# Performance work log

Measured on AMD Instinct MI355X. Metric: run time of the kernel, lower is better.

Reference implementation:

```python
import jax, jax.numpy as jnp
import numpy as np

N_NODES = 20000
N_EDGES = 320000
L = 512   # input feature dim (size_dict['small'][0])
D = 256   # hidden dim (feat_channel), heads=1 so head_dim = 256
C = 2     # n_classes


def setup_inputs() -> dict:
    key = jax.random.key(0)
    ks = jax.random.split(key, 18)
    s = 0.02
    inp = {
        "x": jax.random.normal(ks[0], (N_NODES, L), jnp.float32),
        "edge_index": jax.random.randint(ks[1], (2, N_EDGES), 0, N_NODES, dtype=jnp.int32),
        "label": 1,
        # TransformerConv(L, D, heads=1): query/key/value + root skip projections
        "Wq": jax.random.normal(ks[2], (L, D), jnp.float32) * s,
        "bq": jax.random.normal(ks[3], (D,), jnp.float32) * s,
        "Wk": jax.random.normal(ks[4], (L, D), jnp.float32) * s,
        "bk": jax.random.normal(ks[5], (D,), jnp.float32) * s,
        "Wv": jax.random.normal(ks[6], (L, D), jnp.float32) * s,
        "bv": jax.random.normal(ks[7], (D,), jnp.float32) * s,
        "Ws": jax.random.normal(ks[8], (L, D), jnp.float32) * s,
        "bs": jax.random.normal(ks[9], (D,), jnp.float32) * s,
        # GlobalAdaptPooling: tanh-MLP attention (heads = n_classes) + per-class classifier
        "Wa1": jax.random.normal(ks[10], (D, D), jnp.float32) * s,
        "ba1": jax.random.normal(ks[11], (D,), jnp.float32) * s,
        "Wa2": jax.random.normal(ks[12], (D, C), jnp.float32) * s,
        "ba2": jax.random.normal(ks[13], (C,), jnp.float32) * s,
        "Wc": jax.random.normal(ks[14], (C, D), jnp.float32) * s,
        "bc": jax.random.normal(ks[15], (C,), jnp.float32) * s,
    }
    return inp


def _forward(x, edge_index, label, Wq, bq, Wk, bk, Wv, bv, Ws, bs, Wa1, ba1, Wa2, ba2, Wc, bc):
    n = x.shape[0]
    src = edge_index[0]  # message source j
    dst = edge_index[1]  # message target i
    # --- TransformerConv (heads=1, concat, root_weight=True) ---
    q = x @ Wq + bq                      # [N, D]
    k = x @ Wk + bk
    v = x @ Wv + bv
    score = jnp.sum(q[dst] * k[src], axis=-1) / jnp.sqrt(jnp.float32(D))  # [E]
    # segment softmax over incoming edges of each target node
    m = jax.ops.segment_max(score, dst, num_segments=n)
    e = jnp.exp(score - m[dst])
    den = jax.ops.segment_sum(e, dst, num_segments=n)
    alpha = e / den[dst]                 # [E]
    agg = jax.ops.segment_sum(alpha[:, None] * v[src], dst, num_segments=n)  # [N, D]
    h = agg + x @ Ws + bs
    # --- act: GELU (torch exact/erf) ---
    h = jax.nn.gelu(h, approximate=False)
    # --- GlobalAdaptPooling: node attention with n_classes heads ---
    scores = jnp.tanh(h @ Wa1 + ba1) @ Wa2 + ba2      # [N, C]
    attn = jax.nn.softmax(scores, axis=0)             # softmax over nodes
    M = attn.T @ h                                    # [C, D] per-class bag embedding
    logits = (jnp.sum(M * Wc, axis=1) + bc)[None, :]  # [1, C]
    Y_prob = jax.nn.softmax(logits, axis=1)
    A = attn[:, label]                                # [N] attention for target class
    return logits, Y_prob, A


def reference(x, edge_index, label, Wq, bq, Wk, bk, Wv, bv, Ws, bs, Wa1, ba1, Wa2, ba2, Wc, bc):
    return _forward(x, edge_index, label, Wq, bq, Wk, bk, Wv, bv, Ws, bs, Wa1, ba1, Wa2, ba2, Wc, bc)
```

## Files before the change

kernel.cpp:

```cpp
#include <hip/hip_runtime.h>
#include <hip/hip_bf16.h>
#include <math.h>

typedef float f32x4_t __attribute__((ext_vector_type(4)));
typedef float f32x2_t __attribute__((ext_vector_type(2)));
typedef __bf16 bf16x8_t __attribute__((ext_vector_type(8)));

__device__ __forceinline__ float bf2f(unsigned int u){
  union { float f; unsigned int i; } x; x.i = u << 16; return x.f;
}
__device__ __forceinline__ unsigned short f2bf(float f){
  unsigned int x = __float_as_uint(f);
  unsigned int r = (x + 0x7fffu + ((x >> 16) & 1u)) >> 16;
  return (unsigned short)r;
}
__device__ __forceinline__ unsigned int pk2bf(float a, float b){
  return (unsigned int)f2bf(a) | ((unsigned int)f2bf(b) << 16);
}
__device__ __forceinline__ int swz4(int r){ return (r ^ (r >> 2) ^ (r >> 4)) & 3; }

__device__ __forceinline__ void unp8s(uint4 w, float* f, float s){
  f[0] = bf2f(w.x & 0xffffu) * s; f[1] = bf2f(w.x >> 16) * s;
  f[2] = bf2f(w.y & 0xffffu) * s; f[3] = bf2f(w.y >> 16) * s;
  f[4] = bf2f(w.z & 0xffffu) * s; f[5] = bf2f(w.z >> 16) * s;
  f[6] = bf2f(w.w & 0xffffu) * s; f[7] = bf2f(w.w >> 16) * s;
}
__device__ __forceinline__ void unpf8(unsigned int w, float* f){
  f32x2_t lo = __builtin_amdgcn_cvt_pk_f32_fp8(w, false);
  f32x2_t hi = __builtin_amdgcn_cvt_pk_f32_fp8(w, true);
  f[0] = lo[0]; f[1] = lo[1]; f[2] = hi[0]; f[3] = hi[1];
}
__device__ __forceinline__ float fast_tanh(float y){
  float e = exp2f(y * 2.8853901817f);
  return 1.0f - 2.0f / (e + 1.0f);
}
__device__ __forceinline__ float fast_gelu(float x){
  float x2 = x * x;
  float u = x * fmaf(0.1029527f, x2, 2.3022339f);
  float e = exp2f(u);
  return x - x / (e + 1.0f);
}

#define GLOAD16(gsrc, ldst) \
  __builtin_amdgcn_global_load_lds((const __attribute__((address_space(1))) unsigned int*)(gsrc), \
                                   (__attribute__((address_space(3))) unsigned int*)(ldst), 16, 0, 0)

__global__ void zero_buf(uint4* __restrict__ p, int n16){
  int i = blockIdx.x * 256 + threadIdx.x;
  if (i < n16) p[i] = make_uint4(0, 0, 0, 0);
}

__global__ void prep(const float* __restrict__ x,
                     const float* __restrict__ Wq, const float* __restrict__ Wk,
                     const float* __restrict__ Wv, const float* __restrict__ Ws,
                     const float* __restrict__ bq, const float* __restrict__ bk,
                     const float* __restrict__ bv, const float* __restrict__ bs,
                     const float* __restrict__ Wa1, const int* __restrict__ ei,
                     unsigned short* __restrict__ xbf, unsigned short* __restrict__ wcatT,
                     float* __restrict__ bcat, unsigned short* __restrict__ wa1T,
                     int* __restrict__ deg, int n, int ne, int nbcv){
  const int b = blockIdx.x, tid = threadIdx.x;
  if (b < 2048){
    int idx = b * 256 + tid;
    int c = idx >> 9, k = idx & 511;
    int sel = c >> 8, cc = c & 255;
    const float* W = (sel == 0) ? Wq : (sel == 1) ? Wk : (sel == 2) ? Wv : Ws;
    int p = ((k >> 3) & 3) ^ swz4(c & 127);
    int dst = c * 512 + (k & ~31) + p * 8 + (k & 7);
    wcatT[dst] = f2bf(W[k * 256 + cc]);
    if (idx < 1024){
      int sel2 = idx >> 8, cc2 = idx & 255;
      const float* B = (sel2 == 0) ? bq : (sel2 == 1) ? bk : (sel2 == 2) ? bv : bs;
      bcat[idx] = B[cc2];
    }
  } else if (b < 2304){
    int idx = (b - 2048) * 256 + tid;
    int c = idx >> 8, k = idx & 255;
    wa1T[idx] = f2bf(Wa1[k * 256 + c]);
  } else if (b < 2304 + nbcv){
    int idx = (b - 2304) * 256 + tid;
    if (idx < n * 64){
      int node = idx >> 6, un = idx & 63;
      int k0 = (un >> 2) * 32, u = un & 3;
      const float* src = x + (size_t)node * 512 + k0 + u * 8;
      float4 f0 = *reinterpret_cast<const float4*>(src);
      float4 f1 = *reinterpret_cast<const float4*>(src + 4);
      uint4 o;
      o.x = pk2bf(f0.x, f0.y); o.y = pk2bf(f0.z, f0.w);
      o.z = pk2bf(f1.x, f1.y); o.w = pk2bf(f1.z, f1.w);
      int p = u ^ swz4(node & 127);
      *reinterpret_cast<uint4*>(xbf + (size_t)node * 512 + k0 + p * 8) = o;
    }
  } else {
    int i = (b - 2304 - nbcv) * 256 + tid;
    if (i < ne) atomicAdd(&deg[ei[ne + i]], 1);
  }
}

__global__ __launch_bounds__(256) void gemm_qkvs(const unsigned short* __restrict__ xbf,
                                                 const unsigned short* __restrict__ wcatT,
                                                 const float* __restrict__ bcat,
                                                 unsigned short* __restrict__ qbf,
                                                 unsigned short* __restrict__ sbf,
                                                 unsigned char* __restrict__ kv8,
                                                 int n_nodes, int mblocks){
  __shared__ __align__(16) unsigned char smem[49152];
  const int tid = threadIdx.x;
  const int lane = tid & 63, wave = tid >> 6;
  const int wm = wave >> 1, wn = wave & 1;
  const int g = (blockIdx.x & 7) * mblocks + (blockIdx.x >> 3);
  const int m_blk = g >> 3, n_blk = g & 7;
  const int m0 = m_blk * 128, n0 = n_blk * 128;
  const int lrow = lane >> 2;
  const int lcol = (lane & 3) * 8;
  const int rA0 = min(m0 + wave * 16 + lrow, n_nodes - 1);
  const int rA1 = min(m0 + (wave + 4) * 16 + lrow, n_nodes - 1);
  const int rB0 = n0 + wave * 16 + lrow;
  const int rB1 = rB0 + 64;
  const int r = lane & 15, q4 = lane >> 4;
  const unsigned short* aG0 = xbf   + (size_t)rA0 * 512 + lcol;
  const unsigned short* aG1 = xbf   + (size_t)rA1 * 512 + lcol;
  const unsigned short* bG0 = wcatT + (size_t)rB0 * 512 + lcol;
  const unsigned short* bG1 = wcatT + (size_t)rB1 * 512 + lcol;
  int aoff[4], boff[4];
  #pragma unroll
  for (int mi = 0; mi < 4; mi++){ int rr = wm * 64 + mi * 16 + r; aoff[mi] = rr * 32 + ((q4 ^ swz4(rr)) * 8); }
  #pragma unroll
  for (int ni = 0; ni < 4; ni++){ int rb = wn * 64 + ni * 16 + r; boff[ni] = rb * 32 + ((q4 ^ swz4(rb)) * 8); }
  f32x4_t acc[4][4] = {};
#define STAGE(base, k0) { \
    unsigned short* As_ = (unsigned short*)(smem + (base)); \
    unsigned short* Bs_ = (unsigned short*)(smem + (base) + 8192); \
    GLOAD16(aG0 + (k0), &As_[wave * 512]); \
    GLOAD16(aG1 + (k0), &As_[(wave + 4) * 512]); \
    GLOAD16(bG0 + (k0), &Bs_[wave * 512]); \
    GLOAD16(bG1 + (k0), &Bs_[(wave + 4) * 512]); \
  }
  STAGE(0, 0);
  STAGE(16384, 32);
  int cbase = 0;
  int sbase = 32768;
  for (int t = 0; t < 16; t++){
    if (t + 2 < 16){
      STAGE(sbase, (t + 2) * 32);
      asm volatile("s_waitcnt vmcnt(8)" ::: "memory");
    } else if (t + 1 < 16){
      asm volatile("s_waitcnt vmcnt(4)" ::: "memory");
    } else {
      asm volatile("s_waitcnt vmcnt(0)" ::: "memory");
    }
    __builtin_amdgcn_s_barrier();
    asm volatile("" ::: "memory");
    const unsigned short* As = (const unsigned short*)(smem + cbase);
    const unsigned short* Bs = (const unsigned short*)(smem + cbase + 8192);
    bf16x8_t a[4], b[4];
    #pragma unroll
    for (int mi = 0; mi < 4; mi++) a[mi] = *reinterpret_cast<const bf16x8_t*>(&As[aoff[mi]]);
    #pragma unroll
    for (int ni = 0; ni < 4; ni++) b[ni] = *reinterpret_cast<const bf16x8_t*>(&Bs[boff[ni]]);
    #pragma unroll
    for (int mi = 0; mi < 4; mi++)
      #pragma unroll
      for (int ni = 0; ni < 4; ni++)
        acc[mi][ni] = __builtin_amdgcn_mfma_f32_16x16x32_bf16(b[ni], a[mi], acc[mi][ni], 0, 0, 0);
    __builtin_amdgcn_s_barrier();
    asm volatile("" ::: "memory");
    cbase += 16384; if (cbase == 49152) cbase = 0;
    sbase += 16384; if (sbase == 49152) sbase = 0;
  }
#undef STAGE
  const bool isQ = (n_blk < 2), isS = (n_blk >= 6);
  if (isQ || isS){
    unsigned short* St = (unsigned short*)smem;
    unsigned short* outp = isQ ? qbf : sbf;
    const int colhalf = isQ ? n_blk : (n_blk - 6);
    #pragma unroll
    for (int ch = 0; ch < 2; ch++){
      if (wm == ch){
        #pragma unroll
        for (int mi = 0; mi < 4; mi++){
          #pragma unroll
          for (int ni = 0; ni < 4; ni++){
            int mloc = mi * 16 + r;
            int nl = wn * 64 + ni * 16 + q4 * 4;
            float4 bb = *reinterpret_cast<const float4*>(&bcat[n0 + nl]);
            uint2 w;
            w.x = pk2bf(acc[mi][ni][0] + bb.x, acc[mi][ni][1] + bb.y);
            w.y = pk2bf(acc[mi][ni][2] + bb.z, acc[mi][ni][3] + bb.w);
            *reinterpret_cast<uint2*>(&St[mloc * 152 + nl]) = w;
          }
        }
      }
      __syncthreads();
      #pragma unroll
      for (int it = 0; it < 4; it++){
        int u = it * 256 + tid;
        int row = u >> 4, seg = (u & 15) * 8;
        int node = m0 + ch * 64 + row;
        if (node < n_nodes){
          uint4 v = *reinterpret_cast<const uint4*>(&St[row * 152 + seg]);
          *reinterpret_cast<uint4*>(outp + (size_t)node * 256 + colhalf * 128 + seg) = v;
        }
      }
      __syncthreads();
    }
  } else {
    unsigned char* St8 = smem;
    #pragma unroll
    for (int ch = 0; ch < 2; ch++){
      if (wm == ch){
        #pragma unroll
        for (int mi = 0; mi < 4; mi++){
          #pragma unroll
          for (int ni = 0; ni < 4; ni++){
            int mloc = mi * 16 + r;
            int nl = wn * 64 + ni * 16 + q4 * 4;
            float4 bb = *reinterpret_cast<const float4*>(&bcat[n0 + nl]);
            int u = 0;
            u = __builtin_amdgcn_cvt_pk_fp8_f32(acc[mi][ni][0] + bb.x, acc[mi][ni][1] + bb.y, u, false);
            u = __builtin_amdgcn_cvt_pk_fp8_f32(acc[mi][ni][2] + bb.z, acc[mi][ni][3] + bb.w, u, true);
            *reinterpret_cast<unsigned int*>(&St8[mloc * 144 + nl]) = (unsigned int)u;
          }
        }
      }
      __syncthreads();
      #pragma unroll
      for (int it = 0; it < 2; it++){
        int u = it * 256 + tid;
        int row = u >> 3, seg = (u & 7) * 16;
        int node = m0 + ch * 64 + row;
        if (node < n_nodes){
          uint4 v = *reinterpret_cast<const uint4*>(&St8[row * 144 + seg]);
          *reinterpret_cast<uint4*>(kv8 + (size_t)node * 512 + (n_blk - 2) * 128 + seg) = v;
        }
      }
      __syncthreads();
    }
  }
}

__global__ void scan_deg(const int* __restrict__ deg, int* __restrict__ rowstart, int n, int ne){
  __shared__ int sm[1024];
  int tid = threadIdx.x;
  int per = (n + 1023) / 1024;
  int start = tid * per;
  int sum = 0;
  for (int i = 0; i < per; i++){
    int idx = start + i;
    sum += (idx < n) ? deg[idx] : 0;
  }
  sm[tid] = sum; __syncthreads();
  for (int off = 1; off < 1024; off <<= 1){
    int t = (tid >= off) ? sm[tid - off] : 0;
    __syncthreads();
    sm[tid] += t;
    __syncthreads();
  }
  int run = sm[tid] - sum;
  for (int i = 0; i < per; i++){
    int idx = start + i;
    if (idx < n){
      rowstart[idx] = run;
      run += deg[idx];
    }
  }
  if (tid == 0) rowstart[n] = ne;
}

__global__ void scatter_edges(const int* __restrict__ ei, const int* __restrict__ rowstart,
                              int* __restrict__ cursor, int* __restrict__ csrsrc, int ne){
  int i = blockIdx.x * 256 + threadIdx.x;
  if (i < ne){
    int d = ei[ne + i];
    int pos = atomicAdd(&cursor[d], 1);
    csrsrc[rowstart[d] + pos] = ei[i] << 9;
  }
}

__global__ __launch_bounds__(256) void edge_attn(const unsigned short* __restrict__ qbf,
                                                 const unsigned short* __restrict__ sbf,
                                                 const unsigned char* __restrict__ kv8,
                                                 const int* __restrict__ rowstart,
                                                 const int* __restrict__ csrsrc,
                                                 unsigned short* __restrict__ hbf, int n_nodes){
  const int tid = threadIdx.x;
  const int lane = tid & 63, wave = tid >> 6;
  const int g = lane >> 4, t = lane & 15;
  const int chain = g & 1;
  const int node = blockIdx.x * 8 + wave * 2 + (g >> 1);
  const bool active = node < n_nodes;
  const int nd = active ? node : 0;
  const float qs = 0.0625f * 1.44269504088896340736f;
  float q[16];
  {
    const unsigned short* qp = qbf + (size_t)nd * 256 + t * 16;
    uint4 w0 = *reinterpret_cast<const uint4*>(qp);
    uint4 w1 = *reinterpret_cast<const uint4*>(qp + 8);
    unp8s(w0, q, qs); unp8s(w1, q + 8, qs);
  }
  int rs = rowstart[nd];
  int re = active ? rowstart[nd + 1] : rs;
  float m = -1e30f, den = 0.f;
  float acc[16];
  #pragma unroll
  for (int j = 0; j < 16; j++) acc[j] = 0.f;
  const int i0 = rs + chain;
  uint4 kA = make_uint4(0,0,0,0), vA = kA, kB = kA, vB = kA;
  if (i0 < re){
    const unsigned char* p1 = kv8 + (size_t)csrsrc[i0] + t * 16;
    kA = *reinterpret_cast<const uint4*>(p1);
    vA = *reinterpret_cast<const uint4*>(p1 + 256);
    if (i0 + 2 < re){
      const unsigned char* p2 = kv8 + (size_t)csrsrc[i0 + 2] + t * 16;
      kB = *reinterpret_cast<const uint4*>(p2);
      vB = *reinterpret_cast<const uint4*>(p2 + 256);
    }
  }
  for (int i = i0; i < re; i += 4){
    uint4 k1 = kA, v1 = vA, k2 = kB, v2 = vB;
    const bool has2 = (i + 2 < re);
    if (i + 4 < re){
      const unsigned char* p1 = kv8 + (size_t)csrsrc[i + 4] + t * 16;
      kA = *reinterpret_cast<const uint4*>(p1);
      vA = *reinterpret_cast<const uint4*>(p1 + 256);
      if (i + 6 < re){
        const unsigned char* p2 = kv8 + (size_t)csrsrc[i + 6] + t * 16;
        kB = *reinterpret_cast<const uint4*>(p2);
        vB = *reinterpret_cast<const uint4*>(p2 + 256);
      }
    }
    float kf1[16], kf2[16];
    unpf8(k1.x, kf1); unpf8(k1.y, kf1 + 4); unpf8(k1.z, kf1 + 8); unpf8(k1.w, kf1 + 12);
    unpf8(k2.x, kf2); unpf8(k2.y, kf2 + 4); unpf8(k2.z, kf2 + 8); unpf8(k2.w, kf2 + 12);
    float s1 = 0.f, s2 = 0.f;
    #pragma unroll
    for (int j = 0; j < 16; j++){ s1 = fmaf(q[j], kf1[j], s1); s2 = fmaf(q[j], kf2[j], s2); }
    s1 += __shfl_xor(s1, 1); s2 += __shfl_xor(s2, 1);
    s1 += __shfl_xor(s1, 2); s2 += __shfl_xor(s2, 2);
    s1 += __shfl_xor(s1, 4); s2 += __shfl_xor(s2, 4);
    s1 += __shfl_xor(s1, 8); s2 += __shfl_xor(s2, 8);
    if (!has2) s2 = -1e30f;
    float vf1[16], vf2[16];
    unpf8(v1.x, vf1); unpf8(v1.y, vf1 + 4); unpf8(v1.z, vf1 + 8); unpf8(v1.w, vf1 + 12);
    unpf8(v2.x, vf2); unpf8(v2.y, vf2 + 4); unpf8(v2.z, vf2 + 8); unpf8(v2.w, vf2 + 12);
    float mn = fmaxf(m, fmaxf(s1, s2));
    float sc = exp2f(m - mn);
    float e1 = exp2f(s1 - mn);
    float e2 = exp2f(s2 - mn);
    den = den * sc + e1 + e2;
    #pragma unroll
    for (int j = 0; j < 16; j++)
      acc[j] = fmaf(acc[j], sc, fmaf(e1, vf1[j], e2 * vf2[j]));
    m = mn;
  }
  {
    float mo  = __shfl_xor(m, 16);
    float dno = __shfl_xor(den, 16);
    float mn  = fmaxf(m, mo);
    float a_  = exp2f(m - mn);
    float b_  = exp2f(mo - mn);
    den = den * a_ + dno * b_;
    #pragma unroll
    for (int j = 0; j < 16; j++){
      float oth = __shfl_xor(acc[j], 16);
      acc[j] = acc[j] * a_ + oth * b_;
    }
  }
  float inv = (den > 0.f) ? 1.f / den : 0.f;
  const unsigned short* sp = sbf + (size_t)nd * 256 + t * 16;
  uint4 s0 = *reinterpret_cast<const uint4*>(sp);
  uint4 s1v = *reinterpret_cast<const uint4*>(sp + 8);
  float sf[16]; unp8s(s0, sf, 1.0f); unp8s(s1v, sf + 8, 1.0f);
  unsigned int o[8];
  #pragma unroll
  for (int j = 0; j < 8; j++){
    float h0 = fast_gelu(acc[2 * j] * inv + sf[2 * j]);
    float h1 = fast_gelu(acc[2 * j + 1] * inv + sf[2 * j + 1]);
    o[j] = (unsigned int)f2bf(h0) | ((unsigned int)f2bf(h1) << 16);
  }
  if (active && chain == 0){
    uint4* dst = reinterpret_cast<uint4*>(hbf + (size_t)node * 256 + t * 16);
    dst[0] = make_uint4(o[0], o[1], o[2], o[3]);
    dst[1] = make_uint4(o[4], o[5], o[6], o[7]);
  }
}

__global__ __launch_bounds__(256) void mlp_mfma(const unsigned short* __restrict__ hbf,
                                                const unsigned short* __restrict__ wa1T,
                                                const float* __restrict__ ba1,
                                                const float* __restrict__ Wa2,
                                                const float* __restrict__ ba2,
                                                float* __restrict__ s2, int n_nodes){
  __shared__ __align__(16) unsigned short As[64 * 72];
  __shared__ float s2s[64][2];
  const int tid = threadIdx.x;
  const int lane = tid & 63, wave = tid >> 6;
  const int m0 = blockIdx.x * 64;
  const int c0 = wave * 64;
  const int r = lane & 15, rg = (lane >> 4) * 4;
  if (tid < 128) s2s[tid >> 1][tid & 1] = 0.f;
  f32x4_t acc[4][4] = {};
  for (int k0 = 0; k0 < 256; k0 += 64){
    int arow = tid >> 2, akc = (tid & 3) * 16;
    uint4 a0v = make_uint4(0,0,0,0), a1v = make_uint4(0,0,0,0);
    if (m0 + arow < n_nodes){
      const unsigned short* src = hbf + (size_t)(m0 + arow) * 256 + k0 + akc;
      a0v = *reinterpret_cast<const uint4*>(src);
      a1v = *reinterpret_cast<const uint4*>(src + 8);
    }
    *reinterpret_cast<uint4*>(&As[arow * 72 + akc]) = a0v;
    *reinterpret_cast<uint4*>(&As[arow * 72 + akc + 8]) = a1v;
    __syncthreads();
    #pragma unroll
    for (int kk = 0; kk < 2; kk++){
      int kg = kk * 32 + (lane >> 4) * 8;
      bf16x8_t a[4], b[4];
      #pragma unroll
      for (int mi = 0; mi < 4; mi++)
        a[mi] = *reinterpret_cast<const bf16x8_t*>(&As[(mi * 16 + r) * 72 + kg]);
      #pragma unroll
      for (int ni = 0; ni < 4; ni++)
        b[ni] = *reinterpret_cast<const bf16x8_t*>(wa1T + (size_t)(c0 + ni * 16 + r) * 256 + k0 + kg);
      #pragma unroll
      for (int mi = 0; mi < 4; mi++)
        #pragma unroll
        for (int ni = 0; ni < 4; ni++)
          acc[mi][ni] = __builtin_amdgcn_mfma_f32_16x16x32_bf16(a[mi], b[ni], acc[mi][ni], 0, 0, 0);
    }
    __syncthreads();
  }
  float w20[4], w21[4], b1c[4];
  #pragma unroll
  for (int ni = 0; ni < 4; ni++){
    int col = c0 + ni * 16 + r;
    w20[ni] = Wa2[col * 2]; w21[ni] = Wa2[col * 2 + 1]; b1c[ni] = ba1[col];
  }
  #pragma unroll
  for (int mi = 0; mi < 4; mi++){
    #pragma unroll
    for (int j = 0; j < 4; j++){
      float t0 = 0.f, t1 = 0.f;
      #pragma unroll
      for (int ni = 0; ni < 4; ni++){
        float t = fast_tanh(acc[mi][ni][j] + b1c[ni]);
        t0 += t * w20[ni]; t1 += t * w21[ni];
      }
      t0 += __shfl_xor(t0, 1); t0 += __shfl_xor(t0, 2);
      t0 += __shfl_xor(t0, 4); t0 += __shfl_xor(t0, 8);
      t1 += __shfl_xor(t1, 1); t1 += __shfl_xor(t1, 2);
      t1 += __shfl_xor(t1, 4); t1 += __shfl_xor(t1, 8);
      if (r == 0){
        int row = mi * 16 + rg + j;
        atomicAdd(&s2s[row][0], t0);
        atomicAdd(&s2s[row][1], t1);
      }
    }
  }
  __syncthreads();
  if (tid < 128){
    int row = tid >> 1, c = tid & 1;
    int node = m0 + row;
    if (node < n_nodes) s2[node * 2 + c] = s2s[row][c] + ba2[c];
  }
}

__global__ void col_reduce(const float* __restrict__ s2, float* __restrict__ red, int n){
  __shared__ float sm[1024];
  __shared__ float mshare[2];
  int tid = threadIdx.x;
  float mx0 = -INFINITY, mx1 = -INFINITY;
  for (int i = tid; i < n; i += 1024){
    mx0 = fmaxf(mx0, s2[2 * i]);
    mx1 = fmaxf(mx1, s2[2 * i + 1]);
  }
  sm[tid] = mx0; __syncthreads();
  for (int off = 512; off > 0; off >>= 1){
    if (tid < off) sm[tid] = fmaxf(sm[tid], sm[tid + off]);
    __syncthreads();
  }
  if (tid == 0) mshare[0] = sm[0];
  __syncthreads();
  sm[tid] = mx1; __syncthreads();
  for (int off = 512; off > 0; off >>= 1){
    if (tid < off) sm[tid] = fmaxf(sm[tid], sm[tid + off]);
    __syncthreads();
  }
  if (tid == 0) mshare[1] = sm[0];
  __syncthreads();
  float m0 = mshare[0], m1 = mshare[1];
  float s0 = 0.f, s1 = 0.f;
  for (int i = tid; i < n; i += 1024){
    s0 += expf(s2[2 * i] - m0);
    s1 += expf(s2[2 * i + 1] - m1);
  }
  sm[tid] = s0; __syncthreads();
  for (int off = 512; off > 0; off >>= 1){
    if (tid < off) sm[tid] += sm[tid + off];
    __syncthreads();
  }
  float den0 = sm[0];
  __syncthreads();
  sm[tid] = s1; __syncthreads();
  for (int off = 512; off > 0; off >>= 1){
    if (tid < off) sm[tid] += sm[tid + off];
    __syncthreads();
  }
  if (tid == 0){
    red[0] = m0; red[1] = m1; red[2] = den0; red[3] = sm[0];
  }
}

__global__ __launch_bounds__(256) void attn_M(const float* __restrict__ s2, const float* __restrict__ red,
                                              const unsigned short* __restrict__ hbf, const int* __restrict__ label,
                                              float* __restrict__ Mbuf, float* __restrict__ outA, int n){
  __shared__ float a0s[256], a1s[256];
  __shared__ float Ms[512];
  int tid = threadIdx.x;
  int n0 = blockIdx.x * 256;
  int node = n0 + tid;
  float m0 = red[0], m1 = red[1];
  float i0 = 1.f / red[2], i1 = 1.f / red[3];
  float a0 = 0.f, a1 = 0.f;
  if (node < n){
    a0 = expf(s2[2 * node] - m0) * i0;
    a1 = expf(s2[2 * node + 1] - m1) * i1;
    outA[node] = (label[0] == 0) ? a0 : a1;
  }
  a0s[tid] = a0; a1s[tid] = a1;
  Ms[tid] = 0.f; Ms[tid + 256] = 0.f;
  __syncthreads();
  const int dgrp = tid & 31;
  const int nl = tid >> 5;
  float M0[8] = {}, M1[8] = {};
  for (int i = nl; i < 256; i += 8){
    int nd = n0 + i;
    if (nd >= n) break;
    uint4 w = *reinterpret_cast<const uint4*>(hbf + (size_t)nd * 256 + dgrp * 8);
    float f[8]; unp8s(w, f, 1.0f);
    float A0 = a0s[i], A1 = a1s[i];
    #pragma unroll
    for (int j = 0; j < 8; j++){
      M0[j] = fmaf(A0, f[j], M0[j]);
      M1[j] = fmaf(A1, f[j], M1[j]);
    }
  }
  #pragma unroll
  for (int j = 0; j < 8; j++){
    M0[j] += __shfl_xor(M0[j], 32);
    M1[j] += __shfl_xor(M1[j], 32);
  }
  if ((tid & 32) == 0){
    #pragma unroll
    for (int j = 0; j < 8; j++){
      atomicAdd(&Ms[dgrp * 8 + j], M0[j]);
      atomicAdd(&Ms[256 + dgrp * 8 + j], M1[j]);
    }
  }
  __syncthreads();
  atomicAdd(&Mbuf[tid], Ms[tid]);
  atomicAdd(&Mbuf[256 + tid], Ms[tid + 256]);
}

__global__ void final_k(const float* __restrict__ Mbuf, const float* __restrict__ Wc,
                        const float* __restrict__ bc, float* __restrict__ out){
  __shared__ float sm[256];
  __shared__ float l0s;
  int tid = threadIdx.x;
  float p0 = Mbuf[tid] * Wc[tid];
  float p1 = Mbuf[256 + tid] * Wc[256 + tid];
  sm[tid] = p0; __syncthreads();
  for (int off = 128; off > 0; off >>= 1){
    if (tid < off) sm[tid] += sm[tid + off];
    __syncthreads();
  }
  if (tid == 0) l0s = sm[0];
  __syncthreads();
  sm[tid] = p1; __syncthreads();
  for (int off = 128; off > 0; off >>= 1){
    if (tid < off) sm[tid] += sm[tid + off];
    __syncthreads();
  }
  if (tid == 0){
    float l0 = l0s + bc[0];
    float l1 = sm[0] + bc[1];
    out[0] = l0; out[1] = l1;
    float mx = fmaxf(l0, l1);
    float e0 = expf(l0 - mx), e1 = expf(l1 - mx);
    float inv = 1.f / (e0 + e1);
    out[2] = e0 * inv; out[3] = e1 * inv;
  }
}

extern "C" void kernel_launch(void* const* d_in, const int* in_sizes, int n_in,
                              void* d_out, int out_size, void* d_ws, size_t ws_size,
                              hipStream_t stream) {
  const float* x   = (const float*)d_in[0];
  const int*   ei  = (const int*)d_in[1];
  const int*   lab = (const int*)d_in[2];
  const float* Wq  = (const float*)d_in[3];
  const float* bq  = (const float*)d_in[4];
  const float* Wk  = (const float*)d_in[5];
  const float* bk  = (const float*)d_in[6];
  const float* Wv  = (const float*)d_in[7];
  const float* bv  = (const float*)d_in[8];
  const float* Ws  = (const float*)d_in[9];
  const float* bs  = (const float*)d_in[10];
  const float* Wa1 = (const float*)d_in[11];
  const float* ba1 = (const float*)d_in[12];
  const float* Wa2 = (const float*)d_in[13];
  const float* ba2 = (const float*)d_in[14];
  const float* Wc  = (const float*)d_in[15];
  const float* bc  = (const float*)d_in[16];
  float* out = (float*)d_out;

  const int n  = in_sizes[0] / 512;
  const int ne = in_sizes[1] / 2;

  char* ws = (char*)d_ws;
  size_t off = 0;
  auto take = [&](size_t bytes){ size_t r = off; off += (bytes + 255) & ~(size_t)255; return r; };
  unsigned short* wcatT  = (unsigned short*)(ws + take((size_t)1024 * 512 * 2));
  float*          bcat   = (float*)(ws + take(1024 * 4));
  unsigned short* xbf    = (unsigned short*)(ws + take((size_t)n * 512 * 2));
  unsigned short* qbf    = (unsigned short*)(ws + take((size_t)n * 256 * 2));
  unsigned short* sbf    = (unsigned short*)(ws + take((size_t)n * 256 * 2));
  unsigned char*  kv8    = (unsigned char*)(ws + take((size_t)n * 512));
  unsigned short* hbf    = (unsigned short*)(ws + take((size_t)n * 256 * 2));
  unsigned short* wa1T   = (unsigned short*)(ws + take((size_t)256 * 256 * 2));
  float*          s2     = (float*)(ws + take((size_t)n * 2 * 4));
  size_t zoff = off;
  int*            deg    = (int*)(ws + take((size_t)n * 4));
  int*            cursor = (int*)(ws + take((size_t)n * 4));
  float*          Mbuf   = (float*)(ws + take(512 * 4));
  size_t zlen = off - zoff;
  int*            rowst  = (int*)(ws + take((size_t)(n + 1) * 4));
  int*            csrsrc = (int*)(ws + take((size_t)ne * 4));
  float*          red    = (float*)(ws + take(4 * 4));

  const int z16 = (int)(zlen / 16);
  zero_buf<<<(z16 + 255) / 256, 256, 0, stream>>>((uint4*)(ws + zoff), z16);

  const int nbcv = (n * 64 + 255) / 256;
  const int nbdh = (ne + 255) / 256;
  prep<<<2304 + nbcv + nbdh, 256, 0, stream>>>(x, Wq, Wk, Wv, Ws, bq, bk, bv, bs, Wa1, ei,
                                               xbf, wcatT, bcat, wa1T, deg, n, ne, nbcv);
  const int mblocks = (n + 127) / 128;
  gemm_qkvs<<<8 * mblocks, 256, 0, stream>>>(xbf, wcatT, bcat, qbf, sbf, kv8, n, mblocks);
  scan_deg<<<1, 1024, 0, stream>>>(deg, rowst, n, ne);
  scatter_edges<<<(ne + 255) / 256, 256, 0, stream>>>(ei, rowst, cursor, csrsrc, ne);
  edge_attn<<<(n + 7) / 8, 256, 0, stream>>>(qbf, sbf, kv8, rowst, csrsrc, hbf, n);
  mlp_mfma<<<(n + 63) / 64, 256, 0, stream>>>(hbf, wa1T, ba1, Wa2, ba2, s2, n);
  col_reduce<<<1, 1024, 0, stream>>>(s2, red, n);
  attn_M<<<(n + 255) / 256, 256, 0, stream>>>(s2, red, hbf, lab, Mbuf, out + 4, n);
  final_k<<<1, 256, 0, stream>>>(Mbuf, Wc, bc, out);
  (void)ws_size; (void)out_size; (void)n_in;
}
```

Baseline: 197.5 us.

## Drop max-subtraction in node softmax and fuse reductions into neighbor kernels

The mlp_mfma epilogue now computes exp of the per-node class scores directly, with no global max, and accumulates the softmax denominators through wave shuffles and global atomics. This removes the single-block col_reduce kernel. The final_k classifier is folded into attn_M with a last-block-done counter, saving two launches and a serial one-block pass. The cost is exp without max-subtraction, which could overflow for large scores (safe here only because the tanh-bounded scores are small), plus atomic and order-dependent summation of the denominators.

```diff
diff --git a/kernel.cpp b/kernel.cpp
--- a/kernel.cpp
+++ b/kernel.cpp
@@ -390,7 +390,8 @@
                                                 const float* __restrict__ ba1,
                                                 const float* __restrict__ Wa2,
                                                 const float* __restrict__ ba2,
-                                                float* __restrict__ s2, int n_nodes){
+                                                float* __restrict__ es2,
+                                                float* __restrict__ den_g, int n_nodes){
   __shared__ __align__(16) unsigned short As[64 * 72];
   __shared__ float s2s[64][2];
   const int tid = threadIdx.x;
@@ -460,70 +461,36 @@
   if (tid < 128){
     int row = tid >> 1, c = tid & 1;
     int node = m0 + row;
-    if (node < n_nodes) s2[node * 2 + c] = s2s[row][c] + ba2[c];
-  }
-}
-
-__global__ void col_reduce(const float* __restrict__ s2, float* __restrict__ red, int n){
-  __shared__ float sm[1024];
-  __shared__ float mshare[2];
-  int tid = threadIdx.x;
-  float mx0 = -INFINITY, mx1 = -INFINITY;
-  for (int i = tid; i < n; i += 1024){
-    mx0 = fmaxf(mx0, s2[2 * i]);
-    mx1 = fmaxf(mx1, s2[2 * i + 1]);
-  }
-  sm[tid] = mx0; __syncthreads();
-  for (int off = 512; off > 0; off >>= 1){
-    if (tid < off) sm[tid] = fmaxf(sm[tid], sm[tid + off]);
-    __syncthreads();
-  }
-  if (tid == 0) mshare[0] = sm[0];
-  __syncthreads();
-  sm[tid] = mx1; __syncthreads();
-  for (int off = 512; off > 0; off >>= 1){
-    if (tid < off) sm[tid] = fmaxf(sm[tid], sm[tid + off]);
-    __syncthreads();
-  }
-  if (tid == 0) mshare[1] = sm[0];
-  __syncthreads();
-  float m0 = mshare[0], m1 = mshare[1];
-  float s0 = 0.f, s1 = 0.f;
-  for (int i = tid; i < n; i += 1024){
-    s0 += expf(s2[2 * i] - m0);
-    s1 += expf(s2[2 * i + 1] - m1);
-  }
-  sm[tid] = s0; __syncthreads();
-  for (int off = 512; off > 0; off >>= 1){
-    if (tid < off) sm[tid] += sm[tid + off];
-    __syncthreads();
-  }
-  float den0 = sm[0];
-  __syncthreads();
-  sm[tid] = s1; __syncthreads();
-  for (int off = 512; off > 0; off >>= 1){
-    if (tid < off) sm[tid] += sm[tid + off];
-    __syncthreads();
-  }
-  if (tid == 0){
-    red[0] = m0; red[1] = m1; red[2] = den0; red[3] = sm[0];
-  }
-}
-
-__global__ __launch_bounds__(256) void attn_M(const float* __restrict__ s2, const float* __restrict__ red,
+    float e = 0.f;
+    if (node < n_nodes){
+      e = expf(s2s[row][c] + ba2[c]);
+      es2[node * 2 + c] = e;
+    }
+    float sum = e;
+    sum += __shfl_xor(sum, 2);  sum += __shfl_xor(sum, 4);
+    sum += __shfl_xor(sum, 8);  sum += __shfl_xor(sum, 16);
+    sum += __shfl_xor(sum, 32);
+    if ((tid & 63) < 2) atomicAdd(&den_g[c], sum);
+  }
+}
+
+__global__ __launch_bounds__(256) void attn_M(const float* __restrict__ es2, const float* __restrict__ den_g,
                                               const unsigned short* __restrict__ hbf, const int* __restrict__ label,
-                                              float* __restrict__ Mbuf, float* __restrict__ outA, int n){
+                                              float* __restrict__ Mbuf, float* __restrict__ outA,
+                                              const float* __restrict__ Wc, const float* __restrict__ bc,
+                                              float* __restrict__ out, unsigned int* __restrict__ cnt,
+                                              int n, int nblocks){
   __shared__ float a0s[256], a1s[256];
   __shared__ float Ms[512];
+  __shared__ unsigned int lastrank;
   int tid = threadIdx.x;
   int n0 = blockIdx.x * 256;
   int node = n0 + tid;
-  float m0 = red[0], m1 = red[1];
-  float i0 = 1.f / red[2], i1 = 1.f / red[3];
+  float i0 = 1.f / den_g[0], i1 = 1.f / den_g[1];
   float a0 = 0.f, a1 = 0.f;
   if (node < n){
-    a0 = expf(s2[2 * node] - m0) * i0;
-    a1 = expf(s2[2 * node + 1] - m1) * i1;
+    a0 = es2[2 * node] * i0;
+    a1 = es2[2 * node + 1] * i1;
     outA[node] = (label[0] == 0) ? a0 : a1;
   }
   a0s[tid] = a0; a1s[tid] = a1;
@@ -559,35 +526,28 @@
   __syncthreads();
   atomicAdd(&Mbuf[tid], Ms[tid]);
   atomicAdd(&Mbuf[256 + tid], Ms[tid + 256]);
-}
-
-__global__ void final_k(const float* __restrict__ Mbuf, const float* __restrict__ Wc,
-                        const float* __restrict__ bc, float* __restrict__ out){
-  __shared__ float sm[256];
-  __shared__ float l0s;
-  int tid = threadIdx.x;
-  float p0 = Mbuf[tid] * Wc[tid];
-  float p1 = Mbuf[256 + tid] * Wc[256 + tid];
-  sm[tid] = p0; __syncthreads();
-  for (int off = 128; off > 0; off >>= 1){
-    if (tid < off) sm[tid] += sm[tid + off];
+  __threadfence();
+  if (tid == 0) lastrank = atomicAdd(cnt, 1u);
+  __syncthreads();
+  if (lastrank == (unsigned int)(nblocks - 1)){
+    float m0v = __hip_atomic_load(&Mbuf[tid], __ATOMIC_RELAXED, __HIP_MEMORY_SCOPE_AGENT);
+    float m1v = __hip_atomic_load(&Mbuf[256 + tid], __ATOMIC_RELAXED, __HIP_MEMORY_SCOPE_AGENT);
+    a0s[tid] = m0v * Wc[tid];
+    a1s[tid] = m1v * Wc[256 + tid];
     __syncthreads();
-  }
-  if (tid == 0) l0s = sm[0];
-  __syncthreads();
-  sm[tid] = p1; __syncthreads();
-  for (int off = 128; off > 0; off >>= 1){
-    if (tid < off) sm[tid] += sm[tid + off];
-    __syncthreads();
-  }
-  if (tid == 0){
-    float l0 = l0s + bc[0];
-    float l1 = sm[0] + bc[1];
-    out[0] = l0; out[1] = l1;
-    float mx = fmaxf(l0, l1);
-    float e0 = expf(l0 - mx), e1 = expf(l1 - mx);
-    float inv = 1.f / (e0 + e1);
-    out[2] = e0 * inv; out[3] = e1 * inv;
+    for (int off = 128; off > 0; off >>= 1){
+      if (tid < off){ a0s[tid] += a0s[tid + off]; a1s[tid] += a1s[tid + off]; }
+      __syncthreads();
+    }
+    if (tid == 0){
+      float l0 = a0s[0] + bc[0];
+      float l1 = a1s[0] + bc[1];
+      out[0] = l0; out[1] = l1;
+      float mx = fmaxf(l0, l1);
+      float e0 = expf(l0 - mx), e1 = expf(l1 - mx);
+      float inv = 1.f / (e0 + e1);
+      out[2] = e0 * inv; out[3] = e1 * inv;
+    }
   }
 }
 
@@ -627,15 +587,16 @@
   unsigned char*  kv8    = (unsigned char*)(ws + take((size_t)n * 512));
   unsigned short* hbf    = (unsigned short*)(ws + take((size_t)n * 256 * 2));
   unsigned short* wa1T   = (unsigned short*)(ws + take((size_t)256 * 256 * 2));
-  float*          s2     = (float*)(ws + take((size_t)n * 2 * 4));
+  float*          es2    = (float*)(ws + take((size_t)n * 2 * 4));
   size_t zoff = off;
   int*            deg    = (int*)(ws + take((size_t)n * 4));
   int*            cursor = (int*)(ws + take((size_t)n * 4));
   float*          Mbuf   = (float*)(ws + take(512 * 4));
+  float*          den_g  = (float*)(ws + take(2 * 4));
+  unsigned int*   cnt    = (unsigned int*)(ws + take(4));
   size_t zlen = off - zoff;
   int*            rowst  = (int*)(ws + take((size_t)(n + 1) * 4));
   int*            csrsrc = (int*)(ws + take((size_t)ne * 4));
-  float*          red    = (float*)(ws + take(4 * 4));
 
   const int z16 = (int)(zlen / 16);
   zero_buf<<<(z16 + 255) / 256, 256, 0, stream>>>((uint4*)(ws + zoff), z16);
@@ -649,9 +610,8 @@
   scan_deg<<<1, 1024, 0, stream>>>(deg, rowst, n, ne);
   scatter_edges<<<(ne + 255) / 256, 256, 0, stream>>>(ei, rowst, cursor, csrsrc, ne);
   edge_attn<<<(n + 7) / 8, 256, 0, stream>>>(qbf, sbf, kv8, rowst, csrsrc, hbf, n);
-  mlp_mfma<<<(n + 63) / 64, 256, 0, stream>>>(hbf, wa1T, ba1, Wa2, ba2, s2, n);
-  col_reduce<<<1, 1024, 0, stream>>>(s2, red, n);
-  attn_M<<<(n + 255) / 256, 256, 0, stream>>>(s2, red, hbf, lab, Mbuf, out + 4, n);
-  final_k<<<1, 256, 0, stream>>>(Mbuf, Wc, bc, out);
+  mlp_mfma<<<(n + 63) / 64, 256, 0, stream>>>(hbf, wa1T, ba1, Wa2, ba2, es2, den_g, n);
+  const int nbam = (n + 255) / 256;
+  attn_M<<<nbam, 256, 0, stream>>>(es2, den_g, hbf, lab, Mbuf, out + 4, Wc, bc, out, cnt, n, nbam);
   (void)ws_size; (void)out_size; (void)n_in;
 }
```

Measured after the change: 189.7 us. 4.0% less time.
